# Optimization experiments

Hardware: AMD Instinct MI355X
Metric: run time of the kernel (lower is better)

Reference implementation:

```python
import jax, jax.numpy as jnp
import numpy as np

EPS = 1e-5
N, M, ORIG, NBR, F, H, N0 = 100000, 12, 92, 41, 64, 128, 2000


def _bn(x, gamma, beta):
    # BatchNorm1d in training mode: biased batch stats over axis 0
    mu = jnp.mean(x, axis=0)
    var = jnp.var(x, axis=0)
    return (x - mu) * jax.lax.rsqrt(var + EPS) * gamma + beta


def _conv_layer(a, nbr, idx, W, b, g1, bt1, g2, bt2):
    n, m = idx.shape
    f = a.shape[1]
    a_nbr = a[idx]  # (N, M, F) gather
    tot = jnp.concatenate(
        [jnp.broadcast_to(a[:, None, :], (n, m, f)), a_nbr, nbr], axis=2
    )  # (N, M, 2F + nbr_fea_len)
    gated = (tot @ W + b).reshape(n * m, 2 * f)
    gated = _bn(gated, g1, bt1).reshape(n, m, 2 * f)
    filt, core = jnp.split(gated, 2, axis=2)
    summed = jnp.sum(jax.nn.sigmoid(filt) * jax.nn.softplus(core), axis=1)  # (N, F)
    summed = _bn(summed, g2, bt2)
    return jax.nn.softplus(a + summed)


def setup_inputs() -> dict:
    key = jax.random.key(0)
    ks = jax.random.split(key, 24)
    s = lambda shape, k, scale=0.05: jax.random.normal(k, shape, jnp.float32) * scale
    inp = {
        "atom_fea": jax.random.normal(ks[0], (N, ORIG), jnp.float32),
        "nbr_fea": jax.random.normal(ks[1], (N, M, NBR), jnp.float32),
        "nbr_fea_idx": jax.random.randint(ks[2], (N, M), 0, N),
        "crystal_id": jnp.sort(jax.random.randint(ks[3], (N,), 0, N0)),
        # embedding
        "W_emb": s((ORIG, F), ks[4]), "b_emb": s((F,), ks[5]),
        # conv layer
        "cW": s((2 * F + NBR, 2 * F), ks[6]), "cb": s((2 * F,), ks[7]),
        "cg1": jnp.ones((2 * F,), jnp.float32), "cbt1": jnp.zeros((2 * F,), jnp.float32),
        "cg2": jnp.ones((F,), jnp.float32), "cbt2": jnp.zeros((F,), jnp.float32),
        # residual block conv layer
        "rW": s((2 * F + NBR, 2 * F), ks[8]), "rb": s((2 * F,), ks[9]),
        "rg1": jnp.ones((2 * F,), jnp.float32), "rbt1": jnp.zeros((2 * F,), jnp.float32),
        "rg2": jnp.ones((F,), jnp.float32), "rbt2": jnp.zeros((F,), jnp.float32),
        # head
        "W_fc": s((F, H), ks[10]), "b_fc": s((H,), ks[11]),
        "W_out": s((H, 1), ks[12]), "b_out": s((1,), ks[13]),
    }
    return inp


def reference(atom_fea, nbr_fea, nbr_fea_idx, crystal_id,
              W_emb, b_emb, cW, cb, cg1, cbt1, cg2, cbt2,
              rW, rb, rg1, rbt1, rg2, rbt2, W_fc, b_fc, W_out, b_out):
    a = atom_fea @ W_emb + b_emb  # (N, F)
    a1 = _conv_layer(a, nbr_fea, nbr_fea_idx, cW, cb, cg1, cbt1, cg2, cbt2)
    # Res_block: softplus(conv(a1) + a1)
    a2 = jax.nn.softplus(
        _conv_layer(a1, nbr_fea, nbr_fea_idx, rW, rb, rg1, rbt1, rg2, rbt2) + a1
    )
    # per-crystal mean pooling (segment mean)
    cnt = jax.ops.segment_sum(jnp.ones((a2.shape[0],), a2.dtype), crystal_id, N0)
    crys = jax.ops.segment_sum(a2, crystal_id, N0) / jnp.maximum(cnt, 1.0)[:, None]
    crys = jax.nn.softplus(jax.nn.softplus(crys) @ W_fc + b_fc)
    return crys @ W_out + b_out  # (N0, 1)
```

## Files before the change

### kernel.cpp

```cpp
#include <hip/hip_runtime.h>
#include <hip/hip_bf16.h>

namespace {

constexpr int N    = 100000;
constexpr int M    = 12;
constexpr int ORIG = 92;
constexpr int NBR  = 41;
constexpr int F    = 64;
constexpr int H    = 128;
constexpr int N0   = 2000;
constexpr float EPS = 1e-5f;

constexpr int NBLK2 = N / 32;

typedef __attribute__((ext_vector_type(8))) short bf16x8;
typedef __attribute__((ext_vector_type(4))) float f32x4;
typedef float f32x4u __attribute__((ext_vector_type(4), aligned(4)));

__device__ __forceinline__ float u2f(unsigned u){ float f; __builtin_memcpy(&f, &u, 4); return f; }

__device__ __forceinline__ float softplusf(float x){
  float t = __expf(-fabsf(x));
  return fmaxf(x, 0.f) + 0.693147180559945f * __log2f(1.f + t);
}
__device__ __forceinline__ float sigmoidf(float x){
  return __fdividef(1.f, 1.f + __expf(-x));
}
__device__ __forceinline__ unsigned short f2bf(float f){
  __hip_bfloat16 h = __float2bfloat16(f);
  unsigned short u; __builtin_memcpy(&u, &h, 2); return u;
}
__device__ __forceinline__ unsigned packbf2(float lo, float hi){
  __hip_bfloat162 b2 = __float22bfloat162_rn(make_float2(lo, hi));
  unsigned u; __builtin_memcpy(&u, &b2, 4); return u;
}
__device__ __forceinline__ void cvt2(bf16x8& d, int e, float a, float b){
  unsigned u = packbf2(a, b);
  d[e]   = (short)(u & 0xffffu);
  d[e+1] = (short)(u >> 16);
}

__global__ void k_embed(const float* __restrict__ af, const float* __restrict__ W,
                        const float* __restrict__ b, float* __restrict__ a){
  __shared__ float row[4][ORIG];
  int base = blockIdx.x * 4;
  for(int t = threadIdx.x; t < 4*ORIG; t += 256){
    row[t/ORIG][t%ORIG] = af[(size_t)(base + t/ORIG)*ORIG + (t%ORIG)];
  }
  __syncthreads();
  int i = base + (threadIdx.x >> 6);
  int j = threadIdx.x & 63;
  const float* r = row[threadIdx.x >> 6];
  float acc = b[j];
  #pragma unroll
  for(int k = 0; k < ORIG; k++) acc = fmaf(r[k], W[k*F + j], acc);
  a[(size_t)i*F + j] = acc;
}

__global__ void k_nbrcvt(const float* __restrict__ nbr, unsigned short* __restrict__ NB){
  const long long total = (long long)(N/16)*M*16*6;
  long long stride = (long long)gridDim.x * blockDim.x;
  for(long long c = (long long)blockIdx.x*blockDim.x + threadIdx.x; c < total; c += stride){
    int seg = (int)(c % 6);
    long long t3 = c / 6;
    int r = (int)(t3 % 16);
    long long t4 = t3 / 16;
    int m = (int)(t4 % M);
    long long atile = t4 / M;
    const float* src = nbr + (((size_t)(atile*16 + r)*M + m)*NBR) + seg*8;
    bf16x8 o = {0,0,0,0,0,0,0,0};
    if(seg < 5){
      f32x4u v0 = *(const f32x4u*)src;
      f32x4u v1 = *(const f32x4u*)(src + 4);
      cvt2(o, 0, v0.x, v0.y); cvt2(o, 2, v0.z, v0.w);
      cvt2(o, 4, v1.x, v1.y); cvt2(o, 6, v1.z, v1.w);
    } else {
      o[0] = (short)f2bf(src[0]);
    }
    *(bf16x8*)(NB + c*8) = o;
  }
}

__global__ void k_prep(const float* __restrict__ W,
                       unsigned short* __restrict__ webf,
                       unsigned short* __restrict__ wspf){
  int b = blockIdx.x;
  int l = threadIdx.x, lr = l & 15, lg = l >> 4;
  if(b < 16){
    int ct = b >> 1, s = b & 1;
    unsigned short* dst = webf + ((size_t)b*64 + l)*8;
    #pragma unroll
    for(int e = 0; e < 8; ++e){
      int k = s*32 + lg*8 + e;
      float w = (k < NBR) ? W[(size_t)(128 + k)*128 + ct*16 + lr] : 0.f;
      dst[e] = f2bf(w);
    }
  } else {
    int f = b - 16;
    int ct = f >> 1, ks = f & 1;
    int col = ct*16 + lr;
    unsigned short* dst = wspf + ((size_t)f*64 + l)*8;
    #pragma unroll
    for(int e = 0; e < 8; ++e){
      int k = ks*32 + lg*8 + e;
      float w = (col < 128) ? W[(size_t)k*128 + col]
                            : W[(size_t)(64 + k)*128 + (col - 128)];
      dst[e] = f2bf(w);
    }
  }
}

__global__ __launch_bounds__(256, 3)
void k_spmm(const float* __restrict__ X, const unsigned short* __restrict__ wspf,
            const float* __restrict__ bias,
            unsigned* __restrict__ SU, unsigned long long* __restrict__ Q){
  const int tid = threadIdx.x;
  const int l = tid & 63, lr = l & 15, lg = l >> 4;
  const int w = tid >> 6;
  const int a0 = blockIdx.x * 32;
  const bf16x8* wv = (const bf16x8*)wspf;

  bf16x8 A[2][2];
  #pragma unroll
  for(int t = 0; t < 2; ++t){
    const float* xr = X + (size_t)(a0 + t*16 + lr)*64;
    #pragma unroll
    for(int ks = 0; ks < 2; ++ks){
      f32x4u v0 = *(const f32x4u*)(xr + ks*32 + lg*8);
      f32x4u v1 = *(const f32x4u*)(xr + ks*32 + lg*8 + 4);
      cvt2(A[t][ks], 0, v0.x, v0.y); cvt2(A[t][ks], 2, v0.z, v0.w);
      cvt2(A[t][ks], 4, v1.x, v1.y); cvt2(A[t][ks], 6, v1.z, v1.w);
    }
  }

  const bool isS = (w < 2);
  const int hh = isS ? w : (w - 2);
  int tl[4];
  if(isS){ tl[0] = 2*w; tl[1] = 2*w + 1; tl[2] = 4 + 2*w; tl[3] = 5 + 2*w; }
  else   { tl[0] = 8 + 2*hh; tl[1] = 9 + 2*hh; tl[2] = 12 + 2*hh; tl[3] = 13 + 2*hh; }

  bf16x8 B[4][2];
  #pragma unroll
  for(int ct = 0; ct < 4; ++ct)
    #pragma unroll
    for(int ks = 0; ks < 2; ++ks)
      B[ct][ks] = wv[((size_t)tl[ct]*2 + ks)*64 + l];

  f32x4 D[2][4];
  #pragma unroll
  for(int t = 0; t < 2; ++t)
    #pragma unroll
    for(int ct = 0; ct < 4; ++ct){
      f32x4 z = {0.f,0.f,0.f,0.f};
      z = __builtin_amdgcn_mfma_f32_16x16x32_bf16(A[t][0], B[ct][0], z, 0, 0, 0);
      z = __builtin_amdgcn_mfma_f32_16x16x32_bf16(A[t][1], B[ct][1], z, 0, 0, 0);
      D[t][ct] = z;
    }

  if(isS){
    float blo[2], bhi[2];
    #pragma unroll
    for(int ct = 0; ct < 2; ++ct){
      blo[ct] = bias[32*w + ct*16 + lr];
      bhi[ct] = bias[64 + 32*w + ct*16 + lr];
    }
    #pragma unroll
    for(int t = 0; t < 2; ++t)
      #pragma unroll
      for(int r = 0; r < 4; ++r){
        size_t row = a0 + t*16 + lg*4 + r;
        #pragma unroll
        for(int ct = 0; ct < 2; ++ct)
          SU[row*64 + 32*w + ct*16 + lr] =
            packbf2(D[t][ct][r] + blo[ct], D[t][2 + ct][r] + bhi[ct]);
      }
  } else {
    #pragma unroll
    for(int t = 0; t < 2; ++t)
      #pragma unroll
      for(int r = 0; r < 4; ++r){
        size_t row = a0 + t*16 + lg*4 + r;
        unsigned p0 = packbf2(D[t][0][r], D[t][2][r]);
        unsigned p1 = packbf2(D[t][1][r], D[t][3][r]);
        Q[row*32 + hh*16 + lr] = ((unsigned long long)p1 << 32) | p0;
      }
  }
}

template<int MODE, int NBF>
__global__ __launch_bounds__(256, 4)
void k_pass2(const unsigned* __restrict__ SU, const unsigned long long* __restrict__ Q,
             const float* __restrict__ nbr, const unsigned short* __restrict__ NB,
             const int* __restrict__ idx, const unsigned short* __restrict__ webf,
             const float* __restrict__ sc1, const float* __restrict__ sh1,
             float* __restrict__ SUMb, float* __restrict__ part){
  const int tid = threadIdx.x;
  const int l = tid & 63, lr = l & 15, lg = l >> 4;
  const int wid = tid >> 6, tw = wid >> 1, h = wid & 1;
  const int a0 = blockIdx.x*32 + tw*16;

  bf16x8 Bf[4][2];
  const bf16x8* wv = (const bf16x8*)webf;
  #pragma unroll
  for(int c = 0; c < 4; ++c){
    int cg = (c < 2) ? (2*h + c) : (4 + 2*h + (c - 2));
    Bf[c][0] = wv[(cg*2 + 0)*64 + l];
    Bf[c][1] = wv[(cg*2 + 1)*64 + l];
  }

  unsigned SDu[2][4];
  #pragma unroll
  for(int fc = 0; fc < 2; ++fc)
    #pragma unroll
    for(int r = 0; r < 4; ++r)
      SDu[fc][r] = SU[(size_t)(a0 + lg*4 + r)*64 + h*32 + fc*16 + lr];

  __shared__ int six[32*M];
  for(int u = tid; u < 32*M; u += 256) six[u] = idx[(size_t)blockIdx.x*32*M + u];
  __syncthreads();

  float c1f[2], h1f[2], c1c[2], h1c[2];
  if(MODE == 1){
    #pragma unroll
    for(int fc = 0; fc < 2; ++fc){
      int j = h*32 + fc*16 + lr;
      c1f[fc] = sc1[j];      h1f[fc] = sh1[j];
      c1c[fc] = sc1[64 + j]; h1c[fc] = sh1[64 + j];
    }
  }

  float sg[4] = {0,0,0,0}, ssg[4] = {0,0,0,0};
  float sact[4][2];
  #pragma unroll
  for(int r = 0; r < 4; ++r){ sact[r][0] = 0.f; sact[r][1] = 0.f; }

  const unsigned short* nb_tile;
  const float* fbase;
  if constexpr(NBF) nb_tile = NB + (size_t)(blockIdx.x*2 + tw)*M*768;
  else              fbase = nbr + (size_t)(a0 + lr)*M*NBR;

  #define LOAD_A(mm, A0o, A1o)                                              \
    do{                                                                     \
      if constexpr(NBF){                                                    \
        const unsigned short* nrow = nb_tile + (size_t)(mm)*768 + lr*48;    \
        A0o = *(const bf16x8*)(nrow + lg*8);                                \
        if(lg < 2) A1o = *(const bf16x8*)(nrow + 32 + lg*8);                \
        else       A1o = (bf16x8){0,0,0,0,0,0,0,0};                         \
      } else {                                                              \
        const float* nrow = fbase + (size_t)(mm)*NBR;                       \
        f32x4u v0 = *(const f32x4u*)(nrow + lg*8);                          \
        f32x4u v1 = *(const f32x4u*)(nrow + lg*8 + 4);                      \
        cvt2(A0o, 0, v0.x, v0.y); cvt2(A0o, 2, v0.z, v0.w);                 \
        cvt2(A0o, 4, v1.x, v1.y); cvt2(A0o, 6, v1.z, v1.w);                 \
        A1o = (bf16x8){0,0,0,0,0,0,0,0};                                    \
        if(lg == 0){                                                        \
          f32x4u w0 = *(const f32x4u*)(nrow + 32);                          \
          f32x4u w1 = *(const f32x4u*)(nrow + 36);                          \
          cvt2(A1o, 0, w0.x, w0.y); cvt2(A1o, 2, w0.z, w0.w);               \
          cvt2(A1o, 4, w1.x, w1.y); cvt2(A1o, 6, w1.z, w1.w);               \
        } else if(lg == 1){                                                 \
          A1o[0] = (short)f2bf(nrow[40]);                                   \
        }                                                                   \
      }                                                                     \
    }while(0)

  bf16x8 cA0, cA1, nA0, nA1;
  LOAD_A(0, cA0, cA1);

  #pragma unroll 1
  for(int m = 0; m < M; ++m){
    if(m + 1 < M) LOAD_A(m + 1, nA0, nA1);

    f32x4 D[4];
    #pragma unroll
    for(int c = 0; c < 4; ++c){
      f32x4 z = {0.f,0.f,0.f,0.f};
      z = __builtin_amdgcn_mfma_f32_16x16x32_bf16(cA0, Bf[c][0], z, 0, 0, 0);
      z = __builtin_amdgcn_mfma_f32_16x16x32_bf16(cA1, Bf[c][1], z, 0, 0, 0);
      D[c] = z;
    }

    #pragma unroll
    for(int r = 0; r < 4; ++r){
      int p = six[(tw*16 + lg*4 + r)*M + m];
      unsigned long long q = Q[(size_t)p*32 + h*16 + lr];
      unsigned pvs[2];
      pvs[0] = (unsigned)(q & 0xffffffffull);
      pvs[1] = (unsigned)(q >> 32);
      #pragma unroll
      for(int fc = 0; fc < 2; ++fc){
        unsigned pv = pvs[fc];
        unsigned sv = SDu[fc][r];
        float gf = D[fc][r]     + u2f(sv << 16)         + u2f(pv << 16);
        float gc = D[2 + fc][r] + u2f(sv & 0xffff0000u) + u2f(pv & 0xffff0000u);
        if(MODE == 0){
          sg[fc]     += gf;  ssg[fc]     = fmaf(gf, gf, ssg[fc]);
          sg[2 + fc] += gc;  ssg[2 + fc] = fmaf(gc, gc, ssg[2 + fc]);
        } else {
          float bf_ = fmaf(gf, c1f[fc], h1f[fc]);
          float bc_ = fmaf(gc, c1c[fc], h1c[fc]);
          sact[r][fc] += sigmoidf(bf_) * softplusf(bc_);
        }
      }
    }
    cA0 = nA0; cA1 = nA1;
  }
  #undef LOAD_A

  if(MODE == 0){
    #pragma unroll
    for(int c = 0; c < 4; ++c){
      sg[c]  += __shfl_xor(sg[c], 16, 64);  sg[c]  += __shfl_xor(sg[c], 32, 64);
      ssg[c] += __shfl_xor(ssg[c], 16, 64); ssg[c] += __shfl_xor(ssg[c], 32, 64);
    }
    if(lg == 0){
      float* pb = part + ((size_t)blockIdx.x*2 + tw)*256;
      #pragma unroll
      for(int c = 0; c < 4; ++c){
        int col = (c < 2) ? (h*32 + c*16 + lr) : (64 + h*32 + (c - 2)*16 + lr);
        pb[col]       = sg[c];
        pb[128 + col] = ssg[c];
      }
    }
  } else {
    float ps[2] = {0,0}, pss[2] = {0,0};
    #pragma unroll
    for(int fc = 0; fc < 2; ++fc){
      #pragma unroll
      for(int r = 0; r < 4; ++r){
        float v = sact[r][fc];
        SUMb[(size_t)(a0 + lg*4 + r)*64 + h*32 + fc*16 + lr] = v;
        ps[fc] += v; pss[fc] = fmaf(v, v, pss[fc]);
      }
      ps[fc]  += __shfl_xor(ps[fc], 16, 64);  ps[fc]  += __shfl_xor(ps[fc], 32, 64);
      pss[fc] += __shfl_xor(pss[fc], 16, 64); pss[fc] += __shfl_xor(pss[fc], 32, 64);
    }
    if(lg == 0){
      float* pb = part + ((size_t)blockIdx.x*2 + tw)*128;
      #pragma unroll
      for(int fc = 0; fc < 2; ++fc){
        int j = h*32 + fc*16 + lr;
        pb[j]      = ps[fc];
        pb[64 + j] = pss[fc];
      }
    }
  }
}

__global__ void k_reduce(const float* __restrict__ part, int nblocks, int width,
                         float* __restrict__ out){
  int col = blockIdx.x;
  float s = 0.f;
  for(int b = threadIdx.x; b < nblocks; b += 256) s += part[(size_t)b*width + col];
  __shared__ float red[256];
  red[threadIdx.x] = s;
  __syncthreads();
  for(int off = 128; off; off >>= 1){
    if(threadIdx.x < off) red[threadIdx.x] += red[threadIdx.x + off];
    __syncthreads();
  }
  if(threadIdx.x == 0) out[col] = red[0];
}

__global__ void k_finalize(const float* __restrict__ red, const float* __restrict__ gamma,
                           const float* __restrict__ beta, float* __restrict__ sc,
                           float* __restrict__ sh, float inv, int nch){
  int j = threadIdx.x;
  if(j < nch){
    float mu  = red[j] * inv;
    float var = fmaxf(red[nch + j] * inv - mu*mu, 0.f);
    float r   = rsqrtf(var + EPS);
    float s   = gamma[j] * r;
    sc[j] = s;
    sh[j] = beta[j] - mu * s;
  }
}

__global__ void k_epi(const float* __restrict__ X, const float* __restrict__ SUMb,
                      const float* __restrict__ sc2, const float* __restrict__ sh2,
                      float* __restrict__ Y, int res){
  int stride = gridDim.x * blockDim.x;
  int total = N*F/4;
  for(int e4 = blockIdx.x * blockDim.x + threadIdx.x; e4 < total; e4 += stride){
    f32x4 x = *(const f32x4*)(X + (size_t)e4*4);
    f32x4 s = *(const f32x4*)(SUMb + (size_t)e4*4);
    int j0 = (e4*4) & 63;
    f32x4 y;
    #pragma unroll
    for(int u = 0; u < 4; ++u){
      float t = softplusf(x[u] + fmaf(s[u], sc2[j0 + u], sh2[j0 + u]));
      y[u] = res ? softplusf(t + x[u]) : t;
    }
    *(f32x4*)(Y + (size_t)e4*4) = y;
  }
}

__global__ void k_pool(const float* __restrict__ A2, const int* __restrict__ cid,
                       float* __restrict__ POOL){
  int c = blockIdx.x;
  int j = threadIdx.x;
  int lo = 0, hi = N;
  while(lo < hi){ int mid = (lo + hi) >> 1; if(cid[mid] < c) lo = mid + 1; else hi = mid; }
  int s0 = lo;
  lo = s0; hi = N;
  while(lo < hi){ int mid = (lo + hi) >> 1; if(cid[mid] < c + 1) lo = mid + 1; else hi = mid; }
  int s1 = lo;
  float s = 0.f;
  for(int i = s0; i < s1; i++) s += A2[(size_t)i*F + j];
  POOL[c*F + j] = s / fmaxf((float)(s1 - s0), 1.f);
}

__global__ void k_head(const float* __restrict__ POOL, const float* __restrict__ Wfc,
                       const float* __restrict__ bfc, const float* __restrict__ Wout,
                       const float* __restrict__ bout, float* __restrict__ out){
  int c = blockIdx.x;
  int t = threadIdx.x;
  __shared__ float spv[F];
  if(t < F) spv[t] = softplusf(POOL[c*F + t]);
  __syncthreads();
  float h = bfc[t];
  #pragma unroll
  for(int k = 0; k < F; k++) h = fmaf(spv[k], Wfc[k*H + t], h);
  h = softplusf(h);
  float v = h * Wout[t];
  #pragma unroll
  for(int off = 32; off; off >>= 1) v += __shfl_down(v, off, 64);
  __shared__ float red[2];
  if((t & 63) == 0) red[t >> 6] = v;
  __syncthreads();
  if(t == 0) out[c] = red[0] + red[1] + bout[0];
}

constexpr size_t OFF_A0   = 0;
constexpr size_t OFF_A1   = 25600000;
constexpr size_t OFF_SUMB = 51200000;
constexpr size_t OFF_SU   = 76800000;
constexpr size_t OFF_Q    = 102400000;
constexpr size_t OFF_POOL = 128000000;
constexpr size_t OFF_SP1  = 128512000;
constexpr size_t OFF_SP2  = 134912000;
constexpr size_t OFF_STAT = 138112000;
constexpr size_t OFF_WEBF = 138120192;
constexpr size_t OFF_WSPF = 138136576;
constexpr size_t OFF_NB   = 138169344;
constexpr size_t WS_NEED_NB = OFF_NB + (size_t)N*M*48*2;

}

extern "C" void kernel_launch(void* const* d_in, const int* in_sizes, int n_in,
                              void* d_out, int out_size, void* d_ws, size_t ws_size,
                              hipStream_t stream){
  const float* atom_fea = (const float*)d_in[0];
  const float* nbr_fea  = (const float*)d_in[1];
  const int*   nbr_idx  = (const int*)d_in[2];
  const int*   cid      = (const int*)d_in[3];
  const float* W_emb = (const float*)d_in[4];
  const float* b_emb = (const float*)d_in[5];
  const float* cW  = (const float*)d_in[6];
  const float* cb  = (const float*)d_in[7];
  const float* cg1 = (const float*)d_in[8];
  const float* cbt1= (const float*)d_in[9];
  const float* cg2 = (const float*)d_in[10];
  const float* cbt2= (const float*)d_in[11];
  const float* rW  = (const float*)d_in[12];
  const float* rb  = (const float*)d_in[13];
  const float* rg1 = (const float*)d_in[14];
  const float* rbt1= (const float*)d_in[15];
  const float* rg2 = (const float*)d_in[16];
  const float* rbt2= (const float*)d_in[17];
  const float* W_fc = (const float*)d_in[18];
  const float* b_fc = (const float*)d_in[19];
  const float* W_out= (const float*)d_in[20];
  const float* b_out= (const float*)d_in[21];
  float* out = (float*)d_out;

  char* ws = (char*)d_ws;
  float*    A0   = (float*)(ws + OFF_A0);
  float*    A1   = (float*)(ws + OFF_A1);
  float*    SUMb = (float*)(ws + OFF_SUMB);
  unsigned* SU   = (unsigned*)(ws + OFF_SU);
  unsigned long long* Q = (unsigned long long*)(ws + OFF_Q);
  float*    POOL = (float*)(ws + OFF_POOL);
  float*    SP1  = (float*)(ws + OFF_SP1);
  float*    SP2  = (float*)(ws + OFF_SP2);
  float*    STAT = (float*)(ws + OFF_STAT);
  unsigned short* WEBf = (unsigned short*)(ws + OFF_WEBF);
  unsigned short* WSPf = (unsigned short*)(ws + OFF_WSPF);
  unsigned short* NB   = (unsigned short*)(ws + OFF_NB);
  float* RED1 = STAT;
  float* RED2 = STAT + 256;
  float* SC1  = STAT + 384;
  float* SH1  = STAT + 512;
  float* SC2  = STAT + 640;
  float* SH2  = STAT + 704;

  const bool use_nb = (ws_size >= WS_NEED_NB);

  k_embed<<<N/4, 256, 0, stream>>>(atom_fea, W_emb, b_emb, A0);
  if(use_nb) k_nbrcvt<<<2048, 256, 0, stream>>>(nbr_fea, NB);

  for(int layer = 0; layer < 2; layer++){
    const float* W   = layer ? rW   : cW;
    const float* bb  = layer ? rb   : cb;
    const float* g1  = layer ? rg1  : cg1;
    const float* bt1 = layer ? rbt1 : cbt1;
    const float* g2  = layer ? rg2  : cg2;
    const float* bt2 = layer ? rbt2 : cbt2;
    const float* X = layer ? A1 : A0;
    float*       Y = layer ? A0 : A1;

    k_prep<<<48, 64, 0, stream>>>(W, WEBf, WSPf);
    k_spmm<<<NBLK2, 256, 0, stream>>>(X, WSPf, bb, SU, Q);
    if(use_nb){
      k_pass2<0,1><<<NBLK2, 256, 0, stream>>>(SU, Q, nbr_fea, NB, nbr_idx,
                                              WEBf, SC1, SH1, nullptr, SP1);
    } else {
      k_pass2<0,0><<<NBLK2, 256, 0, stream>>>(SU, Q, nbr_fea, nullptr, nbr_idx,
                                              WEBf, SC1, SH1, nullptr, SP1);
    }
    k_reduce<<<256, 256, 0, stream>>>(SP1, 2*NBLK2, 256, RED1);
    k_finalize<<<1, 128, 0, stream>>>(RED1, g1, bt1, SC1, SH1, 1.f/(float)(N*M), 128);
    if(use_nb){
      k_pass2<1,1><<<NBLK2, 256, 0, stream>>>(SU, Q, nbr_fea, NB, nbr_idx,
                                              WEBf, SC1, SH1, SUMb, SP2);
    } else {
      k_pass2<1,0><<<NBLK2, 256, 0, stream>>>(SU, Q, nbr_fea, nullptr, nbr_idx,
                                              WEBf, SC1, SH1, SUMb, SP2);
    }
    k_reduce<<<128, 256, 0, stream>>>(SP2, 2*NBLK2, 128, RED2);
    k_finalize<<<1, 128, 0, stream>>>(RED2, g2, bt2, SC2, SH2, 1.f/(float)N, 64);
    k_epi<<<2048, 256, 0, stream>>>(X, SUMb, SC2, SH2, Y, layer);
  }

  k_pool<<<N0, 64, 0, stream>>>(A0, cid, POOL);
  k_head<<<N0, 128, 0, stream>>>(POOL, W_fc, b_fc, W_out, b_out, out);
}
```

Before: 634.7 us.

## Fuse nbr conversion into layer-0 stats pass and merge reduce, finalize, epilogue, pool, head

The standalone neighbor-feature bf16 conversion kernel is removed. Its work now happens inside a new layer-0 statistics kernel that reads the fp32 neighbor features, feeds them straight to the MFMA and writes the bf16 copy for later passes. The separate reduce and finalize kernels are merged into one per-channel kernel. The second layer's epilogue is folded into a combined pool+head kernel, so the final activation array is never written or re-read. Together these cut kernel launches and one full pass over the neighbor tensor and activations, at the cost of an uncoalesced fp32 read inside the stats kernel and more serial work per crystal in pooling.

```diff
diff --git a/kernel.cpp b/kernel.cpp
--- a/kernel.cpp
+++ b/kernel.cpp
@@ -17,6 +17,7 @@
 typedef __attribute__((ext_vector_type(8))) short bf16x8;
 typedef __attribute__((ext_vector_type(4))) float f32x4;
 typedef float f32x4u __attribute__((ext_vector_type(4), aligned(4)));
+typedef unsigned long long u64;
 
 __device__ __forceinline__ float u2f(unsigned u){ float f; __builtin_memcpy(&f, &u, 4); return f; }
 
@@ -56,30 +57,6 @@
   #pragma unroll
   for(int k = 0; k < ORIG; k++) acc = fmaf(r[k], W[k*F + j], acc);
   a[(size_t)i*F + j] = acc;
-}
-
-__global__ void k_nbrcvt(const float* __restrict__ nbr, unsigned short* __restrict__ NB){
-  const long long total = (long long)(N/16)*M*16*6;
-  long long stride = (long long)gridDim.x * blockDim.x;
-  for(long long c = (long long)blockIdx.x*blockDim.x + threadIdx.x; c < total; c += stride){
-    int seg = (int)(c % 6);
-    long long t3 = c / 6;
-    int r = (int)(t3 % 16);
-    long long t4 = t3 / 16;
-    int m = (int)(t4 % M);
-    long long atile = t4 / M;
-    const float* src = nbr + (((size_t)(atile*16 + r)*M + m)*NBR) + seg*8;
-    bf16x8 o = {0,0,0,0,0,0,0,0};
-    if(seg < 5){
-      f32x4u v0 = *(const f32x4u*)src;
-      f32x4u v1 = *(const f32x4u*)(src + 4);
-      cvt2(o, 0, v0.x, v0.y); cvt2(o, 2, v0.z, v0.w);
-      cvt2(o, 4, v1.x, v1.y); cvt2(o, 6, v1.z, v1.w);
-    } else {
-      o[0] = (short)f2bf(src[0]);
-    }
-    *(bf16x8*)(NB + c*8) = o;
-  }
 }
 
 __global__ void k_prep(const float* __restrict__ W,
@@ -114,7 +91,7 @@
 __global__ __launch_bounds__(256, 3)
 void k_spmm(const float* __restrict__ X, const unsigned short* __restrict__ wspf,
             const float* __restrict__ bias,
-            unsigned* __restrict__ SU, unsigned long long* __restrict__ Q){
+            unsigned* __restrict__ SU, u64* __restrict__ Q){
   const int tid = threadIdx.x;
   const int l = tid & 63, lr = l & 15, lg = l >> 4;
   const int w = tid >> 6;
@@ -183,14 +160,116 @@
         size_t row = a0 + t*16 + lg*4 + r;
         unsigned p0 = packbf2(D[t][0][r], D[t][2][r]);
         unsigned p1 = packbf2(D[t][1][r], D[t][3][r]);
-        Q[row*32 + hh*16 + lr] = ((unsigned long long)p1 << 32) | p0;
+        Q[row*32 + hh*16 + lr] = ((u64)p1 << 32) | p0;
       }
+  }
+}
+
+__global__ __launch_bounds__(256, 3)
+void k_statcvt(const unsigned* __restrict__ SU, const u64* __restrict__ Q,
+               const float* __restrict__ nbr, unsigned short* __restrict__ NB,
+               const int* __restrict__ idx, const unsigned short* __restrict__ webf,
+               float* __restrict__ part){
+  const int tid = threadIdx.x;
+  const int l = tid & 63, lr = l & 15, lg = l >> 4;
+  const int wid = tid >> 6, tw = wid >> 1, h = wid & 1;
+  const int a0 = blockIdx.x*32 + tw*16;
+
+  bf16x8 Bf[4][2];
+  const bf16x8* wv = (const bf16x8*)webf;
+  #pragma unroll
+  for(int c = 0; c < 4; ++c){
+    int cg = (c < 2) ? (2*h + c) : (4 + 2*h + (c - 2));
+    Bf[c][0] = wv[(cg*2 + 0)*64 + l];
+    Bf[c][1] = wv[(cg*2 + 1)*64 + l];
+  }
+
+  unsigned SDu[2][4];
+  #pragma unroll
+  for(int fc = 0; fc < 2; ++fc)
+    #pragma unroll
+    for(int r = 0; r < 4; ++r)
+      SDu[fc][r] = SU[(size_t)(a0 + lg*4 + r)*64 + h*32 + fc*16 + lr];
+
+  __shared__ int six[32*M];
+  for(int u = tid; u < 32*M; u += 256) six[u] = idx[(size_t)blockIdx.x*32*M + u];
+  __syncthreads();
+
+  float sg[4] = {0,0,0,0}, ssg[4] = {0,0,0,0};
+
+  const float* fbase = nbr + (size_t)(a0 + lr)*M*NBR;
+  unsigned short* nbt = NB + (size_t)(blockIdx.x*2 + tw)*M*768 + lr*48;
+
+  #pragma unroll 1
+  for(int m = 0; m < M; ++m){
+    const float* nrow = fbase + (size_t)m*NBR;
+    bf16x8 A0v, A1v = {0,0,0,0,0,0,0,0};
+    {
+      f32x4u v0 = *(const f32x4u*)(nrow + lg*8);
+      f32x4u v1 = *(const f32x4u*)(nrow + lg*8 + 4);
+      cvt2(A0v, 0, v0.x, v0.y); cvt2(A0v, 2, v0.z, v0.w);
+      cvt2(A0v, 4, v1.x, v1.y); cvt2(A0v, 6, v1.z, v1.w);
+    }
+    if(lg == 0){
+      f32x4u w0 = *(const f32x4u*)(nrow + 32);
+      f32x4u w1 = *(const f32x4u*)(nrow + 36);
+      cvt2(A1v, 0, w0.x, w0.y); cvt2(A1v, 2, w0.z, w0.w);
+      cvt2(A1v, 4, w1.x, w1.y); cvt2(A1v, 6, w1.z, w1.w);
+    } else if(lg == 1){
+      A1v[0] = (short)f2bf(nrow[40]);
+    }
+    if(h == 0){
+      *(bf16x8*)(nbt + (size_t)m*768 + lg*8) = A0v;
+      if(lg < 2) *(bf16x8*)(nbt + (size_t)m*768 + 32 + lg*8) = A1v;
+    }
+
+    f32x4 D[4];
+    #pragma unroll
+    for(int c = 0; c < 4; ++c){
+      f32x4 z = {0.f,0.f,0.f,0.f};
+      z = __builtin_amdgcn_mfma_f32_16x16x32_bf16(A0v, Bf[c][0], z, 0, 0, 0);
+      z = __builtin_amdgcn_mfma_f32_16x16x32_bf16(A1v, Bf[c][1], z, 0, 0, 0);
+      D[c] = z;
+    }
+
+    #pragma unroll
+    for(int r = 0; r < 4; ++r){
+      int p = six[(tw*16 + lg*4 + r)*M + m];
+      u64 q = Q[(size_t)p*32 + h*16 + lr];
+      unsigned pvs[2];
+      pvs[0] = (unsigned)(q & 0xffffffffull);
+      pvs[1] = (unsigned)(q >> 32);
+      #pragma unroll
+      for(int fc = 0; fc < 2; ++fc){
+        unsigned pv = pvs[fc];
+        unsigned sv = SDu[fc][r];
+        float gf = D[fc][r]     + u2f(sv << 16)         + u2f(pv << 16);
+        float gc = D[2 + fc][r] + u2f(sv & 0xffff0000u) + u2f(pv & 0xffff0000u);
+        sg[fc]     += gf;  ssg[fc]     = fmaf(gf, gf, ssg[fc]);
+        sg[2 + fc] += gc;  ssg[2 + fc] = fmaf(gc, gc, ssg[2 + fc]);
+      }
+    }
+  }
+
+  #pragma unroll
+  for(int c = 0; c < 4; ++c){
+    sg[c]  += __shfl_xor(sg[c], 16, 64);  sg[c]  += __shfl_xor(sg[c], 32, 64);
+    ssg[c] += __shfl_xor(ssg[c], 16, 64); ssg[c] += __shfl_xor(ssg[c], 32, 64);
+  }
+  if(lg == 0){
+    float* pb = part + ((size_t)blockIdx.x*2 + tw)*256;
+    #pragma unroll
+    for(int c = 0; c < 4; ++c){
+      int col = (c < 2) ? (h*32 + c*16 + lr) : (64 + h*32 + (c - 2)*16 + lr);
+      pb[col]       = sg[c];
+      pb[128 + col] = ssg[c];
+    }
   }
 }
 
 template<int MODE, int NBF>
 __global__ __launch_bounds__(256, 4)
-void k_pass2(const unsigned* __restrict__ SU, const unsigned long long* __restrict__ Q,
+void k_pass2(const unsigned* __restrict__ SU, const u64* __restrict__ Q,
              const float* __restrict__ nbr, const unsigned short* __restrict__ NB,
              const int* __restrict__ idx, const unsigned short* __restrict__ webf,
              const float* __restrict__ sc1, const float* __restrict__ sh1,
@@ -284,7 +363,7 @@
     #pragma unroll
     for(int r = 0; r < 4; ++r){
       int p = six[(tw*16 + lg*4 + r)*M + m];
-      unsigned long long q = Q[(size_t)p*32 + h*16 + lr];
+      u64 q = Q[(size_t)p*32 + h*16 + lr];
       unsigned pvs[2];
       pvs[0] = (unsigned)(q & 0xffffffffull);
       pvs[1] = (unsigned)(q >> 32);
@@ -348,38 +427,40 @@
   }
 }
 
-__global__ void k_reduce(const float* __restrict__ part, int nblocks, int width,
-                         float* __restrict__ out){
-  int col = blockIdx.x;
-  float s = 0.f;
-  for(int b = threadIdx.x; b < nblocks; b += 256) s += part[(size_t)b*width + col];
-  __shared__ float red[256];
-  red[threadIdx.x] = s;
+__global__ void k_redfin(const float* __restrict__ part, int nblocks, int width,
+                         int nch, const float* __restrict__ gamma,
+                         const float* __restrict__ beta,
+                         float* __restrict__ sc, float* __restrict__ sh,
+                         float inv){
+  int j = blockIdx.x;
+  float s = 0.f, ss = 0.f;
+  for(int b = threadIdx.x; b < nblocks; b += 256){
+    s  += part[(size_t)b*width + j];
+    ss += part[(size_t)b*width + nch + j];
+  }
+  __shared__ float rs[256], rss[256];
+  rs[threadIdx.x] = s; rss[threadIdx.x] = ss;
   __syncthreads();
   for(int off = 128; off; off >>= 1){
-    if(threadIdx.x < off) red[threadIdx.x] += red[threadIdx.x + off];
+    if(threadIdx.x < off){
+      rs[threadIdx.x]  += rs[threadIdx.x + off];
+      rss[threadIdx.x] += rss[threadIdx.x + off];
+    }
     __syncthreads();
   }
-  if(threadIdx.x == 0) out[col] = red[0];
-}
-
-__global__ void k_finalize(const float* __restrict__ red, const float* __restrict__ gamma,
-                           const float* __restrict__ beta, float* __restrict__ sc,
-                           float* __restrict__ sh, float inv, int nch){
-  int j = threadIdx.x;
-  if(j < nch){
-    float mu  = red[j] * inv;
-    float var = fmaxf(red[nch + j] * inv - mu*mu, 0.f);
+  if(threadIdx.x == 0){
+    float mu  = rs[0] * inv;
+    float var = fmaxf(rss[0] * inv - mu*mu, 0.f);
     float r   = rsqrtf(var + EPS);
-    float s   = gamma[j] * r;
-    sc[j] = s;
-    sh[j] = beta[j] - mu * s;
+    float g   = gamma[j] * r;
+    sc[j] = g;
+    sh[j] = beta[j] - mu * g;
   }
 }
 
 __global__ void k_epi(const float* __restrict__ X, const float* __restrict__ SUMb,
                       const float* __restrict__ sc2, const float* __restrict__ sh2,
-                      float* __restrict__ Y, int res){
+                      float* __restrict__ Y){
   int stride = gridDim.x * blockDim.x;
   int total = N*F/4;
   for(int e4 = blockIdx.x * blockDim.x + threadIdx.x; e4 < total; e4 += stride){
@@ -388,42 +469,50 @@
     int j0 = (e4*4) & 63;
     f32x4 y;
     #pragma unroll
-    for(int u = 0; u < 4; ++u){
-      float t = softplusf(x[u] + fmaf(s[u], sc2[j0 + u], sh2[j0 + u]));
-      y[u] = res ? softplusf(t + x[u]) : t;
-    }
+    for(int u = 0; u < 4; ++u)
+      y[u] = softplusf(x[u] + fmaf(s[u], sc2[j0 + u], sh2[j0 + u]));
     *(f32x4*)(Y + (size_t)e4*4) = y;
   }
 }
 
-__global__ void k_pool(const float* __restrict__ A2, const int* __restrict__ cid,
-                       float* __restrict__ POOL){
+__global__ void k_poolhead(const float* __restrict__ X, const float* __restrict__ SUMb,
+                           const float* __restrict__ sc2, const float* __restrict__ sh2,
+                           const int* __restrict__ cid,
+                           const float* __restrict__ Wfc, const float* __restrict__ bfc,
+                           const float* __restrict__ Wout, const float* __restrict__ bout,
+                           float* __restrict__ out){
   int c = blockIdx.x;
-  int j = threadIdx.x;
+  int t = threadIdx.x;
+  int j = t & 63, half = t >> 6;
+
   int lo = 0, hi = N;
   while(lo < hi){ int mid = (lo + hi) >> 1; if(cid[mid] < c) lo = mid + 1; else hi = mid; }
   int s0 = lo;
   lo = s0; hi = N;
   while(lo < hi){ int mid = (lo + hi) >> 1; if(cid[mid] < c + 1) lo = mid + 1; else hi = mid; }
   int s1 = lo;
-  float s = 0.f;
-  for(int i = s0; i < s1; i++) s += A2[(size_t)i*F + j];
-  POOL[c*F + j] = s / fmaxf((float)(s1 - s0), 1.f);
-}
-
-__global__ void k_head(const float* __restrict__ POOL, const float* __restrict__ Wfc,
-                       const float* __restrict__ bfc, const float* __restrict__ Wout,
-                       const float* __restrict__ bout, float* __restrict__ out){
-  int c = blockIdx.x;
-  int t = threadIdx.x;
+
+  float sc_j = sc2[j], sh_j = sh2[j];
+  float acc = 0.f;
+  for(int i = s0 + half; i < s1; i += 2){
+    float x = X[(size_t)i*F + j];
+    float s = SUMb[(size_t)i*F + j];
+    float tv = softplusf(x + fmaf(s, sc_j, sh_j));
+    acc += softplusf(tv + x);
+  }
+  __shared__ float ps[2][64];
+  ps[half][j] = acc;
+  __syncthreads();
   __shared__ float spv[F];
-  if(t < F) spv[t] = softplusf(POOL[c*F + t]);
+  if(t < 64)
+    spv[t] = softplusf((ps[0][t] + ps[1][t]) / fmaxf((float)(s1 - s0), 1.f));
   __syncthreads();
-  float h = bfc[t];
-  #pragma unroll
-  for(int k = 0; k < F; k++) h = fmaf(spv[k], Wfc[k*H + t], h);
-  h = softplusf(h);
-  float v = h * Wout[t];
+
+  float hsum = bfc[t];
+  #pragma unroll
+  for(int k = 0; k < F; k++) hsum = fmaf(spv[k], Wfc[k*H + t], hsum);
+  hsum = softplusf(hsum);
+  float v = hsum * Wout[t];
   #pragma unroll
   for(int off = 32; off; off >>= 1) v += __shfl_down(v, off, 64);
   __shared__ float red[2];
@@ -437,7 +526,6 @@
 constexpr size_t OFF_SUMB = 51200000;
 constexpr size_t OFF_SU   = 76800000;
 constexpr size_t OFF_Q    = 102400000;
-constexpr size_t OFF_POOL = 128000000;
 constexpr size_t OFF_SP1  = 128512000;
 constexpr size_t OFF_SP2  = 134912000;
 constexpr size_t OFF_STAT = 138112000;
@@ -480,16 +568,13 @@
   float*    A1   = (float*)(ws + OFF_A1);
   float*    SUMb = (float*)(ws + OFF_SUMB);
   unsigned* SU   = (unsigned*)(ws + OFF_SU);
-  unsigned long long* Q = (unsigned long long*)(ws + OFF_Q);
-  float*    POOL = (float*)(ws + OFF_POOL);
+  u64*      Q    = (u64*)(ws + OFF_Q);
   float*    SP1  = (float*)(ws + OFF_SP1);
   float*    SP2  = (float*)(ws + OFF_SP2);
   float*    STAT = (float*)(ws + OFF_STAT);
   unsigned short* WEBf = (unsigned short*)(ws + OFF_WEBF);
   unsigned short* WSPf = (unsigned short*)(ws + OFF_WSPF);
   unsigned short* NB   = (unsigned short*)(ws + OFF_NB);
-  float* RED1 = STAT;
-  float* RED2 = STAT + 256;
   float* SC1  = STAT + 384;
   float* SH1  = STAT + 512;
   float* SC2  = STAT + 640;
@@ -498,7 +583,6 @@
   const bool use_nb = (ws_size >= WS_NEED_NB);
 
   k_embed<<<N/4, 256, 0, stream>>>(atom_fea, W_emb, b_emb, A0);
-  if(use_nb) k_nbrcvt<<<2048, 256, 0, stream>>>(nbr_fea, NB);
 
   for(int layer = 0; layer < 2; layer++){
     const float* W   = layer ? rW   : cW;
@@ -508,19 +592,21 @@
     const float* g2  = layer ? rg2  : cg2;
     const float* bt2 = layer ? rbt2 : cbt2;
     const float* X = layer ? A1 : A0;
-    float*       Y = layer ? A0 : A1;
 
     k_prep<<<48, 64, 0, stream>>>(W, WEBf, WSPf);
     k_spmm<<<NBLK2, 256, 0, stream>>>(X, WSPf, bb, SU, Q);
-    if(use_nb){
+
+    if(layer == 0 && use_nb){
+      k_statcvt<<<NBLK2, 256, 0, stream>>>(SU, Q, nbr_fea, NB, nbr_idx, WEBf, SP1);
+    } else if(use_nb){
       k_pass2<0,1><<<NBLK2, 256, 0, stream>>>(SU, Q, nbr_fea, NB, nbr_idx,
-                                              WEBf, SC1, SH1, nullptr, SP1);
+                                              WEBf, nullptr, nullptr, nullptr, SP1);
     } else {
       k_pass2<0,0><<<NBLK2, 256, 0, stream>>>(SU, Q, nbr_fea, nullptr, nbr_idx,
-                                              WEBf, SC1, SH1, nullptr, SP1);
-    }
-    k_reduce<<<256, 256, 0, stream>>>(SP1, 2*NBLK2, 256, RED1);
-    k_finalize<<<1, 128, 0, stream>>>(RED1, g1, bt1, SC1, SH1, 1.f/(float)(N*M), 128);
+                                              WEBf, nullptr, nullptr, nullptr, SP1);
+    }
+    k_redfin<<<128, 256, 0, stream>>>(SP1, 2*NBLK2, 256, 128, g1, bt1, SC1, SH1,
+                                      1.f/(float)(N*M));
     if(use_nb){
       k_pass2<1,1><<<NBLK2, 256, 0, stream>>>(SU, Q, nbr_fea, NB, nbr_idx,
                                               WEBf, SC1, SH1, SUMb, SP2);
@@ -528,11 +614,12 @@
       k_pass2<1,0><<<NBLK2, 256, 0, stream>>>(SU, Q, nbr_fea, nullptr, nbr_idx,
                                               WEBf, SC1, SH1, SUMb, SP2);
     }
-    k_reduce<<<128, 256, 0, stream>>>(SP2, 2*NBLK2, 128, RED2);
-    k_finalize<<<1, 128, 0, stream>>>(RED2, g2, bt2, SC2, SH2, 1.f/(float)N, 64);
-    k_epi<<<2048, 256, 0, stream>>>(X, SUMb, SC2, SH2, Y, layer);
-  }
-
-  k_pool<<<N0, 64, 0, stream>>>(A0, cid, POOL);
-  k_head<<<N0, 128, 0, stream>>>(POOL, W_fc, b_fc, W_out, b_out, out);
-}
+    k_redfin<<<64, 256, 0, stream>>>(SP2, 2*NBLK2, 128, 64, g2, bt2, SC2, SH2,
+                                     1.f/(float)N);
+    if(layer == 0)
+      k_epi<<<2048, 256, 0, stream>>>(X, SUMb, SC2, SH2, A1);
+  }
+
+  k_poolhead<<<N0, 128, 0, stream>>>(A1, SUMb, SC2, SH2, cid,
+                                     W_fc, b_fc, W_out, b_out, out);
+}
```

Result: faster. 615.8 us (-3.0%).
